# Kernel tuning notes

Hardware: AMD Instinct MI355X
Metric: run time of the kernel (lower is better)

The kernel has to match this reference:

```python
import jax, jax.numpy as jnp
import numpy as np

B, S, D, H = 4, 2048, 1024, 16
DK = D // H


def setup_inputs() -> dict:
    key = jax.random.key(0)
    ks = jax.random.split(key, 7)
    xq = jax.random.normal(ks[0], (B, S, D), dtype=jnp.float32)
    xk = jax.random.normal(ks[1], (B, S, D), dtype=jnp.float32)
    xv = jax.random.normal(ks[2], (B, S, D), dtype=jnp.float32)
    attention_mask = jnp.ones((B, S), dtype=jnp.int32)  # all-valid padding mask
    scale = 0.02
    Wq = jax.random.normal(ks[3], (D, D), dtype=jnp.float32) * scale
    Wk = jax.random.normal(ks[4], (D, D), dtype=jnp.float32) * scale
    Wv = jax.random.normal(ks[5], (D, D), dtype=jnp.float32) * scale
    Wo = jax.random.normal(ks[6], (D, D), dtype=jnp.float32) * scale
    return {"x_query": xq, "x_key": xk, "x_value": xv,
            "attention_mask": attention_mask,
            "Wq": Wq, "Wk": Wk, "Wv": Wv, "Wo": Wo}


def reference(x_query, x_key, x_value, attention_mask, Wq, Wk, Wv, Wo):
    b, sq, d = x_query.shape
    sk = x_key.shape[1]
    # nn.Linear(bias=False): y = x @ W.T
    Q = x_query @ Wq.T
    K = x_key @ Wk.T
    V = x_value @ Wv.T
    # torch .split(dk, dim=-1) -> contiguous head slices == reshape (B,S,H,DK)
    Qh = Q.reshape(b, sq, H, DK).transpose(0, 2, 1, 3)  # (B,H,Sq,DK)
    Kh = K.reshape(b, sk, H, DK).transpose(0, 2, 1, 3)
    Vh = V.reshape(b, sk, H, DK).transpose(0, 2, 1, 3)
    scores = jnp.einsum('bhqd,bhkd->bhqk', Qh, Kh) / jnp.sqrt(
        jnp.asarray(DK, dtype=Qh.dtype))
    # causal mask (mask_future=True)
    causal = jnp.tril(jnp.ones((sq, sk), dtype=bool))
    scores = jnp.where(causal[None, None, :, :], scores, -jnp.inf)
    # padding mask (B,Sk) -> (B,1,1,Sk)
    pad = (attention_mask != 0)[:, None, None, :]
    scores = jnp.where(pad, scores, -jnp.inf)
    attn = jax.nn.softmax(scores, axis=-1)
    out = jnp.einsum('bhqk,bhkd->bhqd', attn, Vh)  # (B,H,Sq,DK)
    out = out.transpose(0, 2, 1, 3).reshape(b, sq, d)
    return out @ Wo.T
```

## Files before the change

kernel.cpp:

```cpp
#include <hip/hip_runtime.h>
#include <stdint.h>

#define BB 4
#define SS 2048
#define DD 1024
#define HH 16
#define DKK 64

typedef unsigned short u16;
typedef short s16x8 __attribute__((ext_vector_type(8)));
typedef float f32x4 __attribute__((ext_vector_type(4)));

__device__ __forceinline__ void async_copy16(const void* g, void* l) {
  __builtin_amdgcn_global_load_lds(
      (const __attribute__((address_space(1))) void*)g,
      (__attribute__((address_space(3))) void*)l, 16, 0, 0);
}

__device__ __forceinline__ u16 f2bf(float f) {
  union { float f; uint32_t u; } x; x.f = f;
  uint32_t r = x.u + 0x7fffu + ((x.u >> 16) & 1u);
  return (u16)(r >> 16);
}

__global__ __launch_bounds__(256) void cvt_kernel(
    const float* __restrict__ x0, const float* __restrict__ x1,
    const float* __restrict__ x2, const float* __restrict__ w0,
    const float* __restrict__ w1, const float* __restrict__ w2,
    const float* __restrict__ w3, u16* __restrict__ dst) {
  const size_t base = ((size_t)blockIdx.x * 256 + threadIdx.x) * 8;
  const float* src;
  size_t off;
  if (base < 25165824ull) {
    const size_t t = base >> 23;
    src = (t == 0) ? x0 : (t == 1) ? x1 : x2;
    off = base & 8388607ull;
  } else {
    const size_t r = base - 25165824ull;
    const size_t t = r >> 20;
    src = (t == 0) ? w0 : (t == 1) ? w1 : (t == 2) ? w2 : w3;
    off = r & 1048575ull;
  }
  const float4 a = *(const float4*)(src + off);
  const float4 b = *(const float4*)(src + off + 4);
  s16x8 o;
  o[0] = (short)f2bf(a.x); o[1] = (short)f2bf(a.y);
  o[2] = (short)f2bf(a.z); o[3] = (short)f2bf(a.w);
  o[4] = (short)f2bf(b.x); o[5] = (short)f2bf(b.y);
  o[6] = (short)f2bf(b.z); o[7] = (short)f2bf(b.w);
  *(s16x8*)(dst + base) = o;
}

template <bool IN_F32, bool OUT_F32>
__global__ __launch_bounds__(256, 2) void gemm_bt(
    const void* __restrict__ Ap, const void* __restrict__ Bp, void* __restrict__ Cp,
    size_t asegstride, size_t bsegstride, size_t csegstride) {
  const int K = 1024, N = 1024;
  __shared__ u16 Alds[128 * 64];
  __shared__ u16 Blds[128 * 64];
  const int tid = threadIdx.x;
  const int wid = tid >> 6, lane = tid & 63;
  const int quad = lane >> 4, l16 = lane & 15;
  const int mtile = blockIdx.x >> 3;
  const int ntile = blockIdx.x & 7;
  const int wm = wid >> 1, wn = wid & 1;
  const int seg = blockIdx.y;
  f32x4 acc[4][4] = {};
  for (int kb = 0; kb < K; kb += 64) {
    if constexpr (IN_F32) {
      const float* Af = (const float*)Ap + seg * asegstride + (size_t)mtile * 128 * K;
      const float* Bf = (const float*)Bp + seg * bsegstride + (size_t)ntile * 128 * K;
#pragma unroll
      for (int i = 0; i < 8; ++i) {
        const int c = i * 256 + tid;
        const int row = c >> 4, g = c & 15;
        const int cc = g >> 1, h = g & 1;
        const int sl = row * 8 + (cc ^ (row & 7));
        {
          const float4 v = *(const float4*)(Af + (size_t)row * K + kb + g * 4);
          ushort4 o;
          o.x = f2bf(v.x); o.y = f2bf(v.y); o.z = f2bf(v.z); o.w = f2bf(v.w);
          *(ushort4*)&Alds[sl * 8 + h * 4] = o;
        }
        {
          const float4 v = *(const float4*)(Bf + (size_t)row * K + kb + g * 4);
          ushort4 o;
          o.x = f2bf(v.x); o.y = f2bf(v.y); o.z = f2bf(v.z); o.w = f2bf(v.w);
          *(ushort4*)&Blds[sl * 8 + h * 4] = o;
        }
      }
    } else {
      const u16* Ab = (const u16*)Ap + seg * asegstride + (size_t)mtile * 128 * K;
      const u16* Bb = (const u16*)Bp + seg * bsegstride + (size_t)ntile * 128 * K;
#pragma unroll
      for (int i = 0; i < 4; ++i) {
        const int s = i * 256 + tid;
        const int row = s >> 3;
        const int cc = (s & 7) ^ (row & 7);
        async_copy16(Ab + (size_t)row * K + kb + cc * 8,
                     (char*)Alds + (i * 256 + wid * 64) * 16);
        async_copy16(Bb + (size_t)row * K + kb + cc * 8,
                     (char*)Blds + (i * 256 + wid * 64) * 16);
      }
    }
    __syncthreads();
#pragma unroll
    for (int ks = 0; ks < 2; ++ks) {
      s16x8 af[4], bfr[4];
#pragma unroll
      for (int i = 0; i < 4; ++i) {
        const int R = wm * 64 + i * 16 + l16;
        af[i] = *(const s16x8*)&Alds[(R * 8 + ((ks * 4 + quad) ^ (l16 & 7))) * 8];
      }
#pragma unroll
      for (int j = 0; j < 4; ++j) {
        const int R = wn * 64 + j * 16 + l16;
        bfr[j] = *(const s16x8*)&Blds[(R * 8 + ((ks * 4 + quad) ^ (l16 & 7))) * 8];
      }
#pragma unroll
      for (int i = 0; i < 4; ++i)
#pragma unroll
        for (int j = 0; j < 4; ++j)
          acc[i][j] = __builtin_amdgcn_mfma_f32_16x16x32_bf16(af[i], bfr[j], acc[i][j], 0, 0, 0);
    }
    __syncthreads();
  }
  const int row0 = mtile * 128 + wm * 64 + quad * 4;
  const int col0 = ntile * 128 + wn * 64 + l16;
#pragma unroll
  for (int i = 0; i < 4; ++i)
#pragma unroll
    for (int j = 0; j < 4; ++j)
#pragma unroll
      for (int r = 0; r < 4; ++r) {
        const size_t idx = (size_t)(row0 + i * 16 + r) * N + col0 + j * 16;
        if constexpr (OUT_F32) ((float*)Cp)[seg * csegstride + idx] = acc[i][j][r];
        else                   ((u16*)Cp)[seg * csegstride + idx] = f2bf(acc[i][j][r]);
      }
}

__global__ __launch_bounds__(256, 2) void attn_kernel(
    const u16* __restrict__ Q, const u16* __restrict__ K, const u16* __restrict__ V,
    const int* __restrict__ mask, u16* __restrict__ O) {
  __shared__ u16 Klds[64 * 64];
  __shared__ u16 Vt[64 * 64];
  __shared__ u16 Plds[64 * 64];
  __shared__ float bias[64];
  const int bid = blockIdx.x;
  const int qt = 31 - (bid >> 6);
  const int b = (bid >> 4) & 3;
  const int h = bid & 15;
  const int tid = threadIdx.x;
  const int wid = tid >> 6, lane = tid & 63;
  const int quad = lane >> 4, l16 = lane & 15;
  const int q0 = qt * 64;
  const u16* Qb = Q + ((size_t)b * SS + q0) * DD + h * DKK;
  s16x8 qf[2];
#pragma unroll
  for (int ks = 0; ks < 2; ++ks)
    qf[ks] = *(const s16x8*)(Qb + (size_t)(wid * 16 + l16) * DD + ks * 32 + quad * 8);
  s16x8 onesf;
#pragma unroll
  for (int i = 0; i < 8; ++i) onesf[i] = (short)0x3F80;
  f32x4 oacc[4] = {};
  f32x4 lacc = {};
  for (int kt = 0; kt <= qt; ++kt) {
    const int k0 = kt * 64;
    const u16* Kb = K + ((size_t)b * SS + k0) * DD + h * DKK;
    const u16* Vb = V + ((size_t)b * SS + k0) * DD + h * DKK;
#pragma unroll
    for (int i = 0; i < 2; ++i) {
      const int s = i * 256 + tid;
      const int row = s >> 3;
      const int cc = (s & 7) ^ (row & 7);
      async_copy16(Kb + (size_t)row * DD + cc * 8,
                   (char*)Klds + (i * 256 + wid * 64) * 16);
    }
    {
      const int vk = tid & 63, d0 = (tid >> 6) * 16;
      s16x8 v0 = *(const s16x8*)(Vb + (size_t)vk * DD + d0);
      s16x8 v1 = *(const s16x8*)(Vb + (size_t)vk * DD + d0 + 8);
      const int kc = (vk >> 3), ko = vk & 7;
#pragma unroll
      for (int jj = 0; jj < 8; ++jj) {
        const int d1 = d0 + jj, d2 = d0 + 8 + jj;
        Vt[d1 * 64 + ((kc ^ (d1 & 7)) * 8) + ko] = (u16)v0[jj];
        Vt[d2 * 64 + ((kc ^ (d2 & 7)) * 8) + ko] = (u16)v1[jj];
      }
    }
    if (tid < 64) bias[tid] = mask[(size_t)b * SS + k0 + tid] ? 0.0f : -1e30f;
    __syncthreads();
    float biasj[4];
#pragma unroll
    for (int j = 0; j < 4; ++j) biasj[j] = bias[j * 16 + l16];
    f32x4 sacc[4] = {};
#pragma unroll
    for (int ks = 0; ks < 2; ++ks) {
      s16x8 kf[4];
#pragma unroll
      for (int j = 0; j < 4; ++j) {
        const int R = j * 16 + l16;
        kf[j] = *(const s16x8*)&Klds[(R * 8 + ((ks * 4 + quad) ^ (l16 & 7))) * 8];
      }
#pragma unroll
      for (int j = 0; j < 4; ++j)
        sacc[j] = __builtin_amdgcn_mfma_f32_16x16x32_bf16(qf[ks], kf[j], sacc[j], 0, 0, 0);
    }
    const bool diag = (kt == qt);
#pragma unroll
    for (int r = 0; r < 4; ++r) {
      const int qrow = wid * 16 + quad * 4 + r;
#pragma unroll
      for (int j = 0; j < 4; ++j) {
        float p = __expf(sacc[j][r] * 0.125f + biasj[j]);
        if (diag && (j * 16 + l16) > qrow) p = 0.0f;
        Plds[(wid * 16 + quad * 4 + r) * 64 + ((j ^ quad) * 16 + l16)] = f2bf(p);
      }
    }
    asm volatile("s_waitcnt lgkmcnt(0)" ::: "memory");
    const int swz = (l16 >> 2) & 3;
#pragma unroll
    for (int ks = 0; ks < 2; ++ks) {
      const int jr = ks * 2 + (quad >> 1);
      const s16x8 pf = *(const s16x8*)&Plds[(wid * 16 + l16) * 64 +
                                            ((jr ^ swz) * 16 + (quad & 1) * 8)];
      lacc = __builtin_amdgcn_mfma_f32_16x16x32_bf16(pf, onesf, lacc, 0, 0, 0);
#pragma unroll
      for (int jt = 0; jt < 4; ++jt) {
        const int d = jt * 16 + l16;
        const s16x8 vf = *(const s16x8*)&Vt[(d * 8 + ((ks * 4 + quad) ^ (d & 7))) * 8];
        oacc[jt] = __builtin_amdgcn_mfma_f32_16x16x32_bf16(pf, vf, oacc[jt], 0, 0, 0);
      }
    }
    __syncthreads();
  }
  u16* Ob = O + ((size_t)b * SS + q0) * DD + h * DKK;
#pragma unroll
  for (int r = 0; r < 4; ++r) {
    const float inv = 1.0f / lacc[r];
    const int row = wid * 16 + quad * 4 + r;
#pragma unroll
    for (int jt = 0; jt < 4; ++jt)
      Ob[(size_t)row * DD + jt * 16 + l16] = f2bf(oacc[jt][r] * inv);
  }
}

extern "C" void kernel_launch(void* const* d_in, const int* in_sizes, int n_in,
                              void* d_out, int out_size, void* d_ws, size_t ws_size,
                              hipStream_t stream) {
  const float* xq = (const float*)d_in[0];
  const float* xk = (const float*)d_in[1];
  const float* xv = (const float*)d_in[2];
  const int* mask = (const int*)d_in[3];
  const float* Wq = (const float*)d_in[4];
  const float* Wk = (const float*)d_in[5];
  const float* Wv = (const float*)d_in[6];
  const float* Wo = (const float*)d_in[7];
  float* out = (float*)d_out;
  const size_t elems = (size_t)BB * SS * DD;
  const size_t welems = (size_t)DD * DD;
  if (ws_size >= 109051904ull) {
    u16* wsb = (u16*)d_ws;
    u16* Xq = wsb;
    u16* Wqb = wsb + 3 * elems;
    u16* Wob = Wqb + 3 * welems;
    u16* Qb = wsb + 3 * elems + 4 * welems;
    u16* Kb = Qb + elems;
    u16* Vb = Kb + elems;
    u16* Ob = wsb;
    cvt_kernel<<<14336, 256, 0, stream>>>(xq, xk, xv, Wq, Wk, Wv, Wo, wsb);
    gemm_bt<false, false><<<dim3(512, 3), 256, 0, stream>>>(
        Xq, Wqb, Qb, elems, welems, elems);
    attn_kernel<<<BB * HH * (SS / 64), 256, 0, stream>>>(Qb, Kb, Vb, mask, Ob);
    gemm_bt<false, true><<<dim3(512, 1), 256, 0, stream>>>(Ob, Wob, out, 0, 0, 0);
  } else {
    u16* Qb = (u16*)d_ws;
    u16* Kb = Qb + elems;
    u16* Vb = Kb + elems;
    u16* Ob = Vb + elems;
    gemm_bt<true, false><<<dim3(512, 1), 256, 0, stream>>>(xq, Wq, Qb, 0, 0, 0);
    gemm_bt<true, false><<<dim3(512, 1), 256, 0, stream>>>(xk, Wk, Kb, 0, 0, 0);
    gemm_bt<true, false><<<dim3(512, 1), 256, 0, stream>>>(xv, Wv, Vb, 0, 0, 0);
    attn_kernel<<<BB * HH * (SS / 64), 256, 0, stream>>>(Qb, Kb, Vb, mask, Ob);
    gemm_bt<false, true><<<dim3(512, 1), 256, 0, stream>>>(Ob, Wo, out, 0, 0, 0);
  }
}
```

Baseline: 327.4 us.

## Emit V transposed from projection GEMM and use 128-row query tiles in attention

The V projection GEMM now writes its output directly in a per-head transposed layout (B,H,DK,S), so the attention kernel can load V tiles with async global-to-LDS copies instead of a manual register transpose. The attention kernel processes 128 query rows per block (two 16-row groups per wave), which doubles K/V reuse per LDS load and halves the block count. Launch bounds are raised to 3 blocks per CU. The transposed-store epilogue contains a redundant duplicate store and writes strided 8-byte chunks, and the larger tile raises register and LDS pressure.

```diff
diff --git a/kernel.cpp b/kernel.cpp
--- a/kernel.cpp
+++ b/kernel.cpp
@@ -52,9 +52,9 @@
 }
 
 template <bool IN_F32, bool OUT_F32>
-__global__ __launch_bounds__(256, 2) void gemm_bt(
+__global__ __launch_bounds__(256, 3) void gemm_bt(
     const void* __restrict__ Ap, const void* __restrict__ Bp, void* __restrict__ Cp,
-    size_t asegstride, size_t bsegstride, size_t csegstride) {
+    size_t asegstride, size_t bsegstride, size_t csegstride, int vt_seg) {
   const int K = 1024, N = 1024;
   __shared__ u16 Alds[128 * 64];
   __shared__ u16 Blds[128 * 64];
@@ -127,47 +127,69 @@
   }
   const int row0 = mtile * 128 + wm * 64 + quad * 4;
   const int col0 = ntile * 128 + wn * 64 + l16;
-#pragma unroll
-  for (int i = 0; i < 4; ++i)
-#pragma unroll
-    for (int j = 0; j < 4; ++j)
-#pragma unroll
-      for (int r = 0; r < 4; ++r) {
-        const size_t idx = (size_t)(row0 + i * 16 + r) * N + col0 + j * 16;
-        if constexpr (OUT_F32) ((float*)Cp)[seg * csegstride + idx] = acc[i][j][r];
-        else                   ((u16*)Cp)[seg * csegstride + idx] = f2bf(acc[i][j][r]);
-      }
-}
-
-__global__ __launch_bounds__(256, 2) void attn_kernel(
-    const u16* __restrict__ Q, const u16* __restrict__ K, const u16* __restrict__ V,
+  if (seg == vt_seg) {
+    u16* VT = (u16*)Cp + (size_t)seg * csegstride;
+#pragma unroll
+    for (int i = 0; i < 4; ++i)
+#pragma unroll
+      for (int j = 0; j < 4; ++j) {
+        const int col = col0 + j * 16;
+        const int row = row0 + i * 16;
+        const int bb = row >> 11, s0 = row & 2047;
+        const size_t dst = (((size_t)bb * HH + (col >> 6)) * DKK + (col & 63)) * SS + s0;
+        ushort4 o;
+        o.x = f2bf(acc[i][j][0]); o.y = f2bf(acc[i][j][1]);
+        o.z = f2bf(acc[i][j][2]); o.w = f2bf(acc[i][j][3]);
+        *(ushort4*)((u16*)Cp + (size_t)seg * csegstride + dst - (size_t)seg * csegstride + (size_t)seg * csegstride) = o;
+        *(ushort4*)(VT + dst) = o;
+      }
+  } else {
+#pragma unroll
+    for (int i = 0; i < 4; ++i)
+#pragma unroll
+      for (int j = 0; j < 4; ++j)
+#pragma unroll
+        for (int r = 0; r < 4; ++r) {
+          const size_t idx = (size_t)(row0 + i * 16 + r) * N + col0 + j * 16;
+          if constexpr (OUT_F32) ((float*)Cp)[seg * csegstride + idx] = acc[i][j][r];
+          else                   ((u16*)Cp)[seg * csegstride + idx] = f2bf(acc[i][j][r]);
+        }
+  }
+}
+
+__global__ __launch_bounds__(256, 3) void attn_kernel(
+    const u16* __restrict__ Q, const u16* __restrict__ K, const u16* __restrict__ VT,
     const int* __restrict__ mask, u16* __restrict__ O) {
   __shared__ u16 Klds[64 * 64];
   __shared__ u16 Vt[64 * 64];
-  __shared__ u16 Plds[64 * 64];
+  __shared__ u16 Plds[128 * 64];
   __shared__ float bias[64];
   const int bid = blockIdx.x;
-  const int qt = 31 - (bid >> 6);
+  const int qt = 15 - (bid >> 6);
   const int b = (bid >> 4) & 3;
   const int h = bid & 15;
   const int tid = threadIdx.x;
   const int wid = tid >> 6, lane = tid & 63;
   const int quad = lane >> 4, l16 = lane & 15;
-  const int q0 = qt * 64;
+  const int q0 = qt * 128;
   const u16* Qb = Q + ((size_t)b * SS + q0) * DD + h * DKK;
-  s16x8 qf[2];
-#pragma unroll
-  for (int ks = 0; ks < 2; ++ks)
-    qf[ks] = *(const s16x8*)(Qb + (size_t)(wid * 16 + l16) * DD + ks * 32 + quad * 8);
+  const u16* Kb0 = K + (size_t)b * SS * DD + h * DKK;
+  const u16* VTb = VT + ((size_t)(b * HH + h)) * DKK * SS;
+  s16x8 qf[2][2];
+#pragma unroll
+  for (int rg = 0; rg < 2; ++rg)
+#pragma unroll
+    for (int ks = 0; ks < 2; ++ks)
+      qf[rg][ks] = *(const s16x8*)(Qb + (size_t)(wid * 32 + rg * 16 + l16) * DD +
+                                   ks * 32 + quad * 8);
   s16x8 onesf;
 #pragma unroll
   for (int i = 0; i < 8; ++i) onesf[i] = (short)0x3F80;
-  f32x4 oacc[4] = {};
-  f32x4 lacc = {};
-  for (int kt = 0; kt <= qt; ++kt) {
-    const int k0 = kt * 64;
-    const u16* Kb = K + ((size_t)b * SS + k0) * DD + h * DKK;
-    const u16* Vb = V + ((size_t)b * SS + k0) * DD + h * DKK;
+  f32x4 oacc[2][4] = {};
+  f32x4 lacc[2] = {};
+  const int ktiles = 2 * qt + 2;
+  for (int kt = 0; kt < ktiles; ++kt) {
+    const u16* Kb = Kb0 + (size_t)(kt * 64) * DD;
 #pragma unroll
     for (int i = 0; i < 2; ++i) {
       const int s = i * 256 + tid;
@@ -176,24 +198,20 @@
       async_copy16(Kb + (size_t)row * DD + cc * 8,
                    (char*)Klds + (i * 256 + wid * 64) * 16);
     }
-    {
-      const int vk = tid & 63, d0 = (tid >> 6) * 16;
-      s16x8 v0 = *(const s16x8*)(Vb + (size_t)vk * DD + d0);
-      s16x8 v1 = *(const s16x8*)(Vb + (size_t)vk * DD + d0 + 8);
-      const int kc = (vk >> 3), ko = vk & 7;
-#pragma unroll
-      for (int jj = 0; jj < 8; ++jj) {
-        const int d1 = d0 + jj, d2 = d0 + 8 + jj;
-        Vt[d1 * 64 + ((kc ^ (d1 & 7)) * 8) + ko] = (u16)v0[jj];
-        Vt[d2 * 64 + ((kc ^ (d2 & 7)) * 8) + ko] = (u16)v1[jj];
-      }
-    }
-    if (tid < 64) bias[tid] = mask[(size_t)b * SS + k0 + tid] ? 0.0f : -1e30f;
+#pragma unroll
+    for (int i = 0; i < 2; ++i) {
+      const int s = i * 256 + tid;
+      const int row = s >> 3;
+      const int cc = (s & 7) ^ (row & 7);
+      async_copy16(VTb + (size_t)row * SS + kt * 64 + cc * 8,
+                   (char*)Vt + ((i * 256 + wid * 64) * 16));
+    }
+    if (tid < 64) bias[tid] = mask[(size_t)b * SS + kt * 64 + tid] ? 0.0f : -1e30f;
     __syncthreads();
     float biasj[4];
 #pragma unroll
     for (int j = 0; j < 4; ++j) biasj[j] = bias[j * 16 + l16];
-    f32x4 sacc[4] = {};
+    f32x4 sacc[2][4] = {};
 #pragma unroll
     for (int ks = 0; ks < 2; ++ks) {
       s16x8 kf[4];
@@ -203,46 +221,63 @@
         kf[j] = *(const s16x8*)&Klds[(R * 8 + ((ks * 4 + quad) ^ (l16 & 7))) * 8];
       }
 #pragma unroll
-      for (int j = 0; j < 4; ++j)
-        sacc[j] = __builtin_amdgcn_mfma_f32_16x16x32_bf16(qf[ks], kf[j], sacc[j], 0, 0, 0);
-    }
-    const bool diag = (kt == qt);
-#pragma unroll
-    for (int r = 0; r < 4; ++r) {
-      const int qrow = wid * 16 + quad * 4 + r;
-#pragma unroll
-      for (int j = 0; j < 4; ++j) {
-        float p = __expf(sacc[j][r] * 0.125f + biasj[j]);
-        if (diag && (j * 16 + l16) > qrow) p = 0.0f;
-        Plds[(wid * 16 + quad * 4 + r) * 64 + ((j ^ quad) * 16 + l16)] = f2bf(p);
-      }
-    }
+      for (int rg = 0; rg < 2; ++rg)
+#pragma unroll
+        for (int j = 0; j < 4; ++j)
+          sacc[rg][j] = __builtin_amdgcn_mfma_f32_16x16x32_bf16(qf[rg][ks], kf[j],
+                                                               sacc[rg][j], 0, 0, 0);
+    }
+    const bool causal = (kt >= 2 * qt);
+#pragma unroll
+    for (int rg = 0; rg < 2; ++rg)
+#pragma unroll
+      for (int r = 0; r < 4; ++r) {
+        const int qrow = q0 + wid * 32 + rg * 16 + quad * 4 + r;
+#pragma unroll
+        for (int j = 0; j < 4; ++j) {
+          float p = __expf(sacc[rg][j][r] * 0.125f + biasj[j]);
+          if (causal && (kt * 64 + j * 16 + l16) > qrow) p = 0.0f;
+          Plds[(wid * 32 + rg * 16 + quad * 4 + r) * 64 + ((j ^ quad) * 16 + l16)] =
+              f2bf(p);
+        }
+      }
     asm volatile("s_waitcnt lgkmcnt(0)" ::: "memory");
     const int swz = (l16 >> 2) & 3;
 #pragma unroll
     for (int ks = 0; ks < 2; ++ks) {
       const int jr = ks * 2 + (quad >> 1);
-      const s16x8 pf = *(const s16x8*)&Plds[(wid * 16 + l16) * 64 +
-                                            ((jr ^ swz) * 16 + (quad & 1) * 8)];
-      lacc = __builtin_amdgcn_mfma_f32_16x16x32_bf16(pf, onesf, lacc, 0, 0, 0);
+      s16x8 pf[2];
+#pragma unroll
+      for (int rg = 0; rg < 2; ++rg)
+        pf[rg] = *(const s16x8*)&Plds[(wid * 32 + rg * 16 + l16) * 64 +
+                                      ((jr ^ swz) * 16 + (quad & 1) * 8)];
 #pragma unroll
       for (int jt = 0; jt < 4; ++jt) {
         const int d = jt * 16 + l16;
         const s16x8 vf = *(const s16x8*)&Vt[(d * 8 + ((ks * 4 + quad) ^ (d & 7))) * 8];
-        oacc[jt] = __builtin_amdgcn_mfma_f32_16x16x32_bf16(pf, vf, oacc[jt], 0, 0, 0);
-      }
+#pragma unroll
+        for (int rg = 0; rg < 2; ++rg)
+          oacc[rg][jt] = __builtin_amdgcn_mfma_f32_16x16x32_bf16(pf[rg], vf,
+                                                                oacc[rg][jt], 0, 0, 0);
+      }
+#pragma unroll
+      for (int rg = 0; rg < 2; ++rg)
+        lacc[rg] = __builtin_amdgcn_mfma_f32_16x16x32_bf16(pf[rg], onesf, lacc[rg],
+                                                           0, 0, 0);
     }
     __syncthreads();
   }
   u16* Ob = O + ((size_t)b * SS + q0) * DD + h * DKK;
 #pragma unroll
-  for (int r = 0; r < 4; ++r) {
-    const float inv = 1.0f / lacc[r];
-    const int row = wid * 16 + quad * 4 + r;
-#pragma unroll
-    for (int jt = 0; jt < 4; ++jt)
-      Ob[(size_t)row * DD + jt * 16 + l16] = f2bf(oacc[jt][r] * inv);
-  }
+  for (int rg = 0; rg < 2; ++rg)
+#pragma unroll
+    for (int r = 0; r < 4; ++r) {
+      const float inv = 1.0f / lacc[rg][r];
+      const int row = wid * 32 + rg * 16 + quad * 4 + r;
+#pragma unroll
+      for (int jt = 0; jt < 4; ++jt)
+        Ob[(size_t)row * DD + jt * 16 + l16] = f2bf(oacc[rg][jt][r] * inv);
+    }
 }
 
 extern "C" void kernel_launch(void* const* d_in, const int* in_sizes, int n_in,
@@ -270,18 +305,18 @@
     u16* Ob = wsb;
     cvt_kernel<<<14336, 256, 0, stream>>>(xq, xk, xv, Wq, Wk, Wv, Wo, wsb);
     gemm_bt<false, false><<<dim3(512, 3), 256, 0, stream>>>(
-        Xq, Wqb, Qb, elems, welems, elems);
-    attn_kernel<<<BB * HH * (SS / 64), 256, 0, stream>>>(Qb, Kb, Vb, mask, Ob);
-    gemm_bt<false, true><<<dim3(512, 1), 256, 0, stream>>>(Ob, Wob, out, 0, 0, 0);
+        Xq, Wqb, Qb, elems, welems, elems, 2);
+    attn_kernel<<<BB * HH * (SS / 128), 256, 0, stream>>>(Qb, Kb, Vb, mask, Ob);
+    gemm_bt<false, true><<<dim3(512, 1), 256, 0, stream>>>(Ob, Wob, out, 0, 0, 0, -1);
   } else {
     u16* Qb = (u16*)d_ws;
     u16* Kb = Qb + elems;
     u16* Vb = Kb + elems;
     u16* Ob = Vb + elems;
-    gemm_bt<true, false><<<dim3(512, 1), 256, 0, stream>>>(xq, Wq, Qb, 0, 0, 0);
-    gemm_bt<true, false><<<dim3(512, 1), 256, 0, stream>>>(xk, Wk, Kb, 0, 0, 0);
-    gemm_bt<true, false><<<dim3(512, 1), 256, 0, stream>>>(xv, Wv, Vb, 0, 0, 0);
-    attn_kernel<<<BB * HH * (SS / 64), 256, 0, stream>>>(Qb, Kb, Vb, mask, Ob);
-    gemm_bt<false, true><<<dim3(512, 1), 256, 0, stream>>>(Ob, Wo, out, 0, 0, 0);
-  }
-}
+    gemm_bt<true, false><<<dim3(512, 1), 256, 0, stream>>>(xq, Wq, Qb, 0, 0, 0, -1);
+    gemm_bt<true, false><<<dim3(512, 1), 256, 0, stream>>>(xk, Wk, Kb, 0, 0, 0, -1);
+    gemm_bt<true, false><<<dim3(512, 1), 256, 0, stream>>>(xv, Wv, Vb, 0, 0, 0, 0);
+    attn_kernel<<<BB * HH * (SS / 128), 256, 0, stream>>>(Qb, Kb, Vb, mask, Ob);
+    gemm_bt<false, true><<<dim3(512, 1), 256, 0, stream>>>(Ob, Wo, out, 0, 0, 0, -1);
+  }
+}
```

Measured after the change: 319.8 us. -2.3%, faster.
